# Performance work log

Hardware: AMD Instinct MI355X
Metric: run time of the kernel (lower is better)

Reference implementation:

```python
import jax, jax.numpy as jnp
import numpy as np

NEG_SLOPE = 0.2


def edge_softmax(logits, dst, num_nodes):
    # logits: [E, H]; softmax over edges grouped by destination node
    m = jax.ops.segment_max(logits, dst, num_segments=num_nodes)
    e = jnp.exp(logits - m[dst])
    s = jax.ops.segment_sum(e, dst, num_segments=num_nodes)
    return e / (s[dst] + 1e-16)


def gat_conv(x, edge_index, Wl, Wr, att, bias, We=None, eattr=None):
    # GATv2-style multi-head conv; heads concatenated. No dropout (eval mode).
    N = x.shape[0]
    H, C = att.shape
    xl = (x @ Wl).reshape(N, H, C)
    xr = (x @ Wr).reshape(N, H, C)
    src, dst = edge_index[0], edge_index[1]
    m = xl[src] + xr[dst]                      # [E, H, C]
    if eattr is not None:
        m = m + (eattr @ We).reshape(-1, H, C)
    logits = jnp.einsum('ehc,hc->eh', jax.nn.leaky_relu(m, NEG_SLOPE), att)
    alpha = edge_softmax(logits, dst, N)       # [E, H]
    out = jax.ops.segment_sum(alpha[..., None] * xl[src], dst, num_segments=N)
    return out.reshape(N, H * C) + bias


def layer_norm(h, gamma, beta, eps=1e-5):
    mu = jnp.mean(h, axis=-1, keepdims=True)
    var = jnp.var(h, axis=-1, keepdims=True)
    return (h - mu) * jax.lax.rsqrt(var + eps) * gamma + beta


def setup_inputs() -> dict:
    key = jax.random.key(0)
    N, E, D = 50000, 500000, 128
    H, C = 16, 8
    ks = jax.random.split(key, 32)
    inp = {
        'x': jax.random.normal(ks[0], (N, D), jnp.float32),
        'edge_index': jax.random.randint(ks[1], (2, E), 0, N),
        'edge_index_d2': jax.random.randint(ks[2], (2, E), 0, N),
        'edge_index_d4': jax.random.randint(ks[3], (2, E // 2), 0, N),
        'edge_index_d8': jax.random.randint(ks[4], (2, E // 4), 0, N),
        'dual_attr': jax.random.normal(ks[5], (E, D), jnp.float32),
        'edge_attr': jax.random.normal(ks[6], (E, D), jnp.float32),
        'oemap_idx': jax.random.randint(ks[7], (400000,), 0, E + 1),
    }
    s = 1.0 / np.sqrt(D)
    i = 8
    for c in (1, 2, 3, 4):
        inp[f'Wl{c}'] = jax.random.normal(ks[i], (D, H * C), jnp.float32) * s; i += 1
        inp[f'Wr{c}'] = jax.random.normal(ks[i], (D, H * C), jnp.float32) * s; i += 1
        inp[f'att{c}'] = jax.random.normal(ks[i], (H, C), jnp.float32) * s; i += 1
        inp[f'b{c}'] = jnp.zeros((H * C,), jnp.float32)
    inp['We1'] = jax.random.normal(ks[i], (D, H * C), jnp.float32) * s; i += 1
    inp['fuse_W'] = jax.random.normal(ks[i], (4 * H * C, D), jnp.float32) / np.sqrt(4 * H * C); i += 1
    inp['fuse_b'] = jnp.zeros((D,), jnp.float32)
    inp['ln_g'] = jnp.ones((2 * D,), jnp.float32)
    inp['ln_b'] = jnp.zeros((2 * D,), jnp.float32)
    inp['mlp_W'] = jax.random.normal(ks[i], (2 * D, D), jnp.float32) / np.sqrt(2 * D); i += 1
    inp['mlp_b'] = jnp.zeros((D,), jnp.float32)
    return inp


def reference(x, edge_index, edge_index_d2, edge_index_d4, edge_index_d8,
              dual_attr, edge_attr, oemap_idx,
              Wl1, Wr1, att1, b1, Wl2, Wr2, att2, b2,
              Wl3, Wr3, att3, b3, Wl4, Wr4, att4, b4,
              We1, fuse_W, fuse_b, ln_g, ln_b, mlp_W, mlp_b):
    x1 = gat_conv(x, edge_index, Wl1, Wr1, att1, b1, We1, dual_attr)
    x2 = gat_conv(x, edge_index_d2, Wl2, Wr2, att2, b2)
    x3 = gat_conv(x, edge_index_d4, Wl3, Wr3, att3, b3)
    x4 = gat_conv(x, edge_index_d8, Wl4, Wr4, att4, b4)
    xf = jnp.concatenate([x1, x2, x3, x4], axis=1) @ fuse_W + fuse_b  # [N, D]
    src, dst = edge_index[0], edge_index[1]
    pair = jnp.concatenate([xf[src], xf[dst]], axis=-1)               # [E, 2D]
    e_out = jax.nn.relu(layer_norm(pair, ln_g, ln_b)) @ mlp_W + mlp_b
    edge_attr_new = edge_attr + e_out
    # Node2EdgeNaiveReplace: pad with ones row, gather via oemap_idx
    padded = jnp.concatenate([edge_attr_new, jnp.ones((1, edge_attr_new.shape[1]), edge_attr_new.dtype)], axis=0)
    dual_out = padded[oemap_idx]
    return (xf, edge_attr_new, dual_out)
```

## Files before the change

### kernel.cpp

```cpp
#include <hip/hip_runtime.h>
#include <cstdint>
#include <cstddef>


#define NEG_SLOPE 0.2f

__device__ __forceinline__ unsigned fenc(float f) {
  unsigned u = __float_as_uint(f);
  return (u & 0x80000000u) ? ~u : (u | 0x80000000u);
}
__device__ __forceinline__ float fdec(unsigned k) {
  unsigned u = (k & 0x80000000u) ? (k & 0x7FFFFFFFu) : ~k;
  return __uint_as_float(u);
}

__global__ __launch_bounds__(128) void gemm_rows8_128(
    const float* __restrict__ A, const float* __restrict__ W,
    const float* __restrict__ biasA, float* __restrict__ out,
    int M, int accumulate)
{
  __shared__ __align__(16) float lds[8 * 128];
  const int t = threadIdx.x;
  const int row0 = blockIdx.x * 8;
#pragma unroll
  for (int r = 0; r < 8; ++r) {
    int row = row0 + r;
    float v = 0.f;
    if (row < M) {
      v = A[(size_t)row * 128 + t];
      if (biasA) v += biasA[t];
    }
    lds[r * 128 + t] = v;
  }
  __syncthreads();
  float acc[8] = {0.f, 0.f, 0.f, 0.f, 0.f, 0.f, 0.f, 0.f};
  for (int k = 0; k < 128; k += 4) {
    float w0 = W[(k + 0) * 128 + t];
    float w1 = W[(k + 1) * 128 + t];
    float w2 = W[(k + 2) * 128 + t];
    float w3 = W[(k + 3) * 128 + t];
#pragma unroll
    for (int r = 0; r < 8; ++r) {
      const float4 v = *(const float4*)&lds[r * 128 + k];
      acc[r] += v.x * w0 + v.y * w1 + v.z * w2 + v.w * w3;
    }
  }
#pragma unroll
  for (int r = 0; r < 8; ++r) {
    int row = row0 + r;
    if (row < M) {
      size_t o = (size_t)row * 128 + t;
      out[o] = accumulate ? (out[o] + acc[r]) : acc[r];
    }
  }
}

__global__ __launch_bounds__(128) void logits_conv1(
    const float* __restrict__ xl, const float* __restrict__ xr,
    const int* __restrict__ src, const int* __restrict__ dst,
    const float* __restrict__ dualA, const float* __restrict__ We,
    const float* __restrict__ att,
    float* __restrict__ ebuf, unsigned* __restrict__ nmax, int E)
{
  __shared__ __align__(16) float lds[16 * 128];
  __shared__ int sidx[16], didx[16];
  const int t = threadIdx.x;
  const int e0 = blockIdx.x * 16;

  for (int r = 0; r < 16; ++r) {
    int e = e0 + r;
    lds[r * 128 + t] = (e < E) ? dualA[(size_t)e * 128 + t] : 0.f;
  }
  if (t < 16) {
    int e = e0 + t;
    sidx[t] = (e < E) ? src[e] : 0;
    didx[t] = (e < E) ? dst[e] : 0;
  }
  __syncthreads();

  float acc[16];
#pragma unroll
  for (int r = 0; r < 16; ++r) acc[r] = 0.f;
  for (int k = 0; k < 128; k += 4) {
    float w0 = We[(k + 0) * 128 + t];
    float w1 = We[(k + 1) * 128 + t];
    float w2 = We[(k + 2) * 128 + t];
    float w3 = We[(k + 3) * 128 + t];
#pragma unroll
    for (int r = 0; r < 16; ++r) {
      const float4 v = *(const float4*)&lds[r * 128 + k];
      acc[r] += v.x * w0 + v.y * w1 + v.z * w2 + v.w * w3;
    }
  }

  const float a_t = att[t];
  const int h = t >> 3;
  for (int r = 0; r < 16; ++r) {
    int e = e0 + r;
    if (e >= E) break;
    float m = acc[r] + xl[(size_t)sidx[r] * 128 + t] + xr[(size_t)didx[r] * 128 + t];
    float lr = (m > 0.f) ? m : NEG_SLOPE * m;
    float v = lr * a_t;
    v += __shfl_down(v, 4, 8);
    v += __shfl_down(v, 2, 8);
    v += __shfl_down(v, 1, 8);
    if ((t & 7) == 0) {
      ebuf[(size_t)e * 16 + h] = v;
      atomicMax(&nmax[(size_t)didx[r] * 16 + h], fenc(v));
    }
  }
}

__global__ __launch_bounds__(128) void logits_plain(
    const float* __restrict__ xl, const float* __restrict__ xr,
    const int* __restrict__ src, const int* __restrict__ dst,
    const float* __restrict__ att,
    float* __restrict__ ebuf, unsigned* __restrict__ nmax, int E)
{
  const int e = blockIdx.x;
  const int t = threadIdx.x;
  const int s = src[e], d = dst[e];
  float m = xl[(size_t)s * 128 + t] + xr[(size_t)d * 128 + t];
  float lr = (m > 0.f) ? m : NEG_SLOPE * m;
  float v = lr * att[t];
  v += __shfl_down(v, 4, 8);
  v += __shfl_down(v, 2, 8);
  v += __shfl_down(v, 1, 8);
  if ((t & 7) == 0) {
    int h = t >> 3;
    ebuf[(size_t)e * 16 + h] = v;
    atomicMax(&nmax[(size_t)d * 16 + h], fenc(v));
  }
}

__global__ __launch_bounds__(256) void exp_sum(
    const int* __restrict__ dst, float* __restrict__ ebuf,
    const unsigned* __restrict__ nmax, float* __restrict__ nsum, int E)
{
  int i = blockIdx.x * 256 + threadIdx.x;
  if (i >= E * 16) return;
  int e = i >> 4, h = i & 15;
  int d = dst[e];
  float m = fdec(nmax[(size_t)d * 16 + h]);
  float ex = expf(ebuf[i] - m);
  ebuf[i] = ex;
  atomicAdd(&nsum[(size_t)d * 16 + h], ex);
}

__global__ __launch_bounds__(256) void aggregate(
    const int* __restrict__ src, const int* __restrict__ dst,
    const float* __restrict__ ebuf, const float* __restrict__ nsum,
    const float* __restrict__ xl, float* __restrict__ xc, int E)
{
  long long i = (long long)blockIdx.x * 256 + threadIdx.x;
  if (i >= (long long)E * 128) return;
  int e = (int)(i >> 7), t = (int)(i & 127), h = t >> 3;
  int s = src[e], d = dst[e];
  float alpha = ebuf[(size_t)e * 16 + h] / (nsum[(size_t)d * 16 + h] + 1e-16f);
  atomicAdd(&xc[(size_t)d * 128 + t], alpha * xl[(size_t)s * 128 + t]);
}

__global__ __launch_bounds__(256) void init_xf(
    float* __restrict__ xf, const float* __restrict__ fb, int total)
{
  int i = blockIdx.x * 256 + threadIdx.x;
  if (i < total) xf[i] = fb[i & 127];
}

__global__ __launch_bounds__(128) void edge_mlp(
    const float* __restrict__ xf,
    const int* __restrict__ src, const int* __restrict__ dst,
    const float* __restrict__ ln_g, const float* __restrict__ ln_b,
    const float* __restrict__ mlpW, const float* __restrict__ mlp_b,
    const float* __restrict__ edge_attr, float* __restrict__ out, int E)
{
  __shared__ __align__(16) float lds[16 * 256];
  __shared__ int sidx[16], didx[16];
  const int t = threadIdx.x;
  const int e0 = blockIdx.x * 16;
  if (t < 16) {
    int e = e0 + t;
    sidx[t] = (e < E) ? src[e] : 0;
    didx[t] = (e < E) ? dst[e] : 0;
  }
  __syncthreads();
  for (int r = 0; r < 16; ++r) {
    int e = e0 + r;
    if (e < E) {
      lds[r * 256 + t]       = xf[(size_t)sidx[r] * 128 + t];
      lds[r * 256 + 128 + t] = xf[(size_t)didx[r] * 128 + t];
    } else {
      lds[r * 256 + t] = 0.f;
      lds[r * 256 + 128 + t] = 0.f;
    }
  }
  __syncthreads();

  {
    const int g = t >> 3, j = t & 7;
    float s = 0.f, sq = 0.f;
    for (int i = 0; i < 32; ++i) {
      float v = lds[g * 256 + j + 8 * i];
      s += v; sq += v * v;
    }
    for (int off = 4; off; off >>= 1) {
      s  += __shfl_down(s,  off, 8);
      sq += __shfl_down(sq, off, 8);
    }
    s  = __shfl(s, 0, 8);
    sq = __shfl(sq, 0, 8);
    float mu = s * (1.f / 256.f);
    float var = sq * (1.f / 256.f) - mu * mu;
    float rs = rsqrtf(var + 1e-5f);
    for (int i = 0; i < 32; ++i) {
      int idx = j + 8 * i;
      float v = lds[g * 256 + idx];
      v = (v - mu) * rs * ln_g[idx] + ln_b[idx];
      lds[g * 256 + idx] = v > 0.f ? v : 0.f;
    }
  }
  __syncthreads();

  float acc[16];
#pragma unroll
  for (int r = 0; r < 16; ++r) acc[r] = 0.f;
  for (int k = 0; k < 256; k += 4) {
    float w0 = mlpW[(k + 0) * 128 + t];
    float w1 = mlpW[(k + 1) * 128 + t];
    float w2 = mlpW[(k + 2) * 128 + t];
    float w3 = mlpW[(k + 3) * 128 + t];
#pragma unroll
    for (int r = 0; r < 16; ++r) {
      const float4 v = *(const float4*)&lds[r * 256 + k];
      acc[r] += v.x * w0 + v.y * w1 + v.z * w2 + v.w * w3;
    }
  }
  const float mb = mlp_b[t];
  for (int r = 0; r < 16; ++r) {
    int e = e0 + r;
    if (e < E)
      out[(size_t)e * 128 + t] = edge_attr[(size_t)e * 128 + t] + acc[r] + mb;
  }
}

__global__ __launch_bounds__(256) void gather_dual(
    const int* __restrict__ idx, const float* __restrict__ ean,
    float* __restrict__ out, int M, int E)
{
  long long i = (long long)blockIdx.x * 256 + threadIdx.x;
  if (i >= (long long)M * 128) return;
  int row = (int)(i >> 7), t = (int)(i & 127);
  int r = idx[row];
  out[i] = (r < E) ? ean[(size_t)r * 128 + t] : 1.0f;
}


extern "C" void kernel_launch(void* const* d_in, const int* in_sizes, int n_in,
                              void* d_out, int out_size, void* d_ws, size_t ws_size,
                              hipStream_t stream)
{
  const float* x         = (const float*)d_in[0];
  const int*   ei[4]     = {(const int*)d_in[1], (const int*)d_in[2],
                            (const int*)d_in[3], (const int*)d_in[4]};
  const float* dual_attr = (const float*)d_in[5];
  const float* edge_attr = (const float*)d_in[6];
  const int*   oemap     = (const int*)d_in[7];
  const float* Wl[4]  = {(const float*)d_in[8],  (const float*)d_in[12],
                         (const float*)d_in[16], (const float*)d_in[20]};
  const float* Wr[4]  = {(const float*)d_in[9],  (const float*)d_in[13],
                         (const float*)d_in[17], (const float*)d_in[21]};
  const float* att[4] = {(const float*)d_in[10], (const float*)d_in[14],
                         (const float*)d_in[18], (const float*)d_in[22]};
  const float* bc[4]  = {(const float*)d_in[11], (const float*)d_in[15],
                         (const float*)d_in[19], (const float*)d_in[23]};
  const float* We1    = (const float*)d_in[24];
  const float* fuse_W = (const float*)d_in[25];
  const float* fuse_b = (const float*)d_in[26];
  const float* ln_g   = (const float*)d_in[27];
  const float* ln_b   = (const float*)d_in[28];
  const float* mlp_W  = (const float*)d_in[29];
  const float* mlp_b  = (const float*)d_in[30];

  const int N  = in_sizes[0] / 128;
  int E[4];
  for (int c = 0; c < 4; ++c) E[c] = in_sizes[1 + c] / 2;
  const int Moe = in_sizes[7];

  float* ws    = (float*)d_ws;
  float* xl    = ws;
  float* xr    = xl + (size_t)N * 128;
  float* xc    = xr + (size_t)N * 128;
  float* ebuf  = xc + (size_t)N * 128;
  unsigned* nmax = (unsigned*)(ebuf + (size_t)E[0] * 16);
  float* nsum  = (float*)(nmax + (size_t)N * 16);

  float* xf      = (float*)d_out;
  float* ean     = xf + (size_t)N * 128;
  float* dualout = ean + (size_t)E[0] * 128;

  const int rowBlocks = (N + 7) / 8;

  init_xf<<<(N * 128 + 255) / 256, 256, 0, stream>>>(xf, fuse_b, N * 128);

  for (int c = 0; c < 4; ++c) {
    const int* src = ei[c];
    const int* dst = ei[c] + E[c];

    gemm_rows8_128<<<rowBlocks, 128, 0, stream>>>(x, Wl[c], nullptr, xl, N, 0);
    gemm_rows8_128<<<rowBlocks, 128, 0, stream>>>(x, Wr[c], nullptr, xr, N, 0);

    hipMemsetAsync(xc,   0, (size_t)N * 128 * sizeof(float), stream);
    hipMemsetAsync(nmax, 0, (size_t)N * 16 * sizeof(unsigned), stream);
    hipMemsetAsync(nsum, 0, (size_t)N * 16 * sizeof(float), stream);

    if (c == 0) {
      logits_conv1<<<(E[c] + 15) / 16, 128, 0, stream>>>(
          xl, xr, src, dst, dual_attr, We1, att[c], ebuf, nmax, E[c]);
    } else {
      logits_plain<<<E[c], 128, 0, stream>>>(
          xl, xr, src, dst, att[c], ebuf, nmax, E[c]);
    }

    exp_sum<<<(E[c] * 16 + 255) / 256, 256, 0, stream>>>(dst, ebuf, nmax, nsum, E[c]);

    aggregate<<<(int)(((long long)E[c] * 128 + 255) / 256), 256, 0, stream>>>(
        src, dst, ebuf, nsum, xl, xc, E[c]);

    gemm_rows8_128<<<rowBlocks, 128, 0, stream>>>(
        xc, fuse_W + (size_t)c * 128 * 128, bc[c], xf, N, 1);
  }

  edge_mlp<<<(E[0] + 15) / 16, 128, 0, stream>>>(
      xf, ei[0], ei[0] + E[0], ln_g, ln_b, mlp_W, mlp_b, edge_attr, ean, E[0]);

  gather_dual<<<(int)(((long long)Moe * 128 + 255) / 256), 256, 0, stream>>>(
      oemap, ean, dualout, Moe, E[0]);
}
```

Measured before the change: 3.748 ms.

## Use split-bf16 MFMA for node GEMMs and edge MLP with prepacked weights

Replaces the scalar FP32 GEMMs (node projections, fuse projection) and the edge MLP with MFMA bf16 kernels. Each value is split into high and low bf16 parts and three MFMAs are accumulated to keep near-FP32 accuracy. Weights are prepacked once per call into the MFMA fragment layout in workspace. The edge MLP now loads gathered rows as float4 and computes LayerNorm per edge with 4 lanes. The cost is three times the MFMA work, an extra pack kernel, and accuracy that is slightly below full FP32.

Measured after the change: 3.202 ms. 1.17x faster.

```diff
diff --git a/kernel.cpp b/kernel.cpp
--- a/kernel.cpp
+++ b/kernel.cpp
@@ -5,6 +5,9 @@
 
 #define NEG_SLOPE 0.2f
 
+typedef __attribute__((ext_vector_type(8))) short short8v;
+typedef __attribute__((ext_vector_type(4))) float f32x4v;
+
 __device__ __forceinline__ unsigned fenc(float f) {
   unsigned u = __float_as_uint(f);
   return (u & 0x80000000u) ? ~u : (u | 0x80000000u);
@@ -14,43 +17,190 @@
   return __uint_as_float(u);
 }
 
-__global__ __launch_bounds__(128) void gemm_rows8_128(
-    const float* __restrict__ A, const float* __restrict__ W,
+__device__ __forceinline__ void cvt_bf16x2(float f, short& h, short& l) {
+  unsigned u = __float_as_uint(f);
+  h = (short)(u >> 16);
+  float fh = __uint_as_float(u & 0xFFFF0000u);
+  l = (short)(__float_as_uint(f - fh) >> 16);
+}
+
+struct PackArgs { const float* w[13]; };
+
+__global__ __launch_bounds__(256) void pack_all(PackArgs pa, short* __restrict__ out)
+{
+  const int seg = blockIdx.y;
+  const int K = (seg == 12) ? 256 : 128;
+  const int total = K * 128;
+  int i = blockIdx.x * 256 + threadIdx.x;
+  if (i >= total) return;
+  int j  = i & 7;
+  int l  = (i >> 3) & 63;
+  int ct = (i >> 9) & 7;
+  int s  = i >> 12;
+  int row = s * 32 + (l >> 4) * 8 + j;
+  int col = ct * 16 + (l & 15);
+  float v = pa.w[seg][row * 128 + col];
+  short h, lo;
+  cvt_bf16x2(v, h, lo);
+  short* oseg = out + (size_t)seg * 32768;
+  oseg[i] = h;
+  oseg[total + i] = lo;
+}
+
+__global__ __launch_bounds__(128) void gemm_mfma_n(
+    const float* __restrict__ A, const short* __restrict__ Wp,
     const float* __restrict__ biasA, float* __restrict__ out,
     int M, int accumulate)
 {
-  __shared__ __align__(16) float lds[8 * 128];
+  __shared__ __align__(16) short Ah[32][136];
+  __shared__ __align__(16) short Al[32][136];
   const int t = threadIdx.x;
-  const int row0 = blockIdx.x * 8;
-#pragma unroll
-  for (int r = 0; r < 8; ++r) {
+  const int row0 = blockIdx.x * 32;
+
+  const int cg = t & 31, rg = t >> 5;
+  float4 b4 = make_float4(0.f, 0.f, 0.f, 0.f);
+  if (biasA) b4 = *(const float4*)&biasA[cg * 4];
+#pragma unroll
+  for (int rr = 0; rr < 8; ++rr) {
+    int r = rr * 4 + rg;
     int row = row0 + r;
-    float v = 0.f;
-    if (row < M) {
-      v = A[(size_t)row * 128 + t];
-      if (biasA) v += biasA[t];
-    }
-    lds[r * 128 + t] = v;
+    float4 v = make_float4(0.f, 0.f, 0.f, 0.f);
+    if (row < M) v = *(const float4*)&A[(size_t)row * 128 + cg * 4];
+    v.x += b4.x; v.y += b4.y; v.z += b4.z; v.w += b4.w;
+    short h0, h1, h2, h3, l0, l1, l2, l3;
+    cvt_bf16x2(v.x, h0, l0); cvt_bf16x2(v.y, h1, l1);
+    cvt_bf16x2(v.z, h2, l2); cvt_bf16x2(v.w, h3, l3);
+    *(short4*)&Ah[r][cg * 4] = make_short4(h0, h1, h2, h3);
+    *(short4*)&Al[r][cg * 4] = make_short4(l0, l1, l2, l3);
   }
   __syncthreads();
-  float acc[8] = {0.f, 0.f, 0.f, 0.f, 0.f, 0.f, 0.f, 0.f};
-  for (int k = 0; k < 128; k += 4) {
-    float w0 = W[(k + 0) * 128 + t];
-    float w1 = W[(k + 1) * 128 + t];
-    float w2 = W[(k + 2) * 128 + t];
-    float w3 = W[(k + 3) * 128 + t];
-#pragma unroll
-    for (int r = 0; r < 8; ++r) {
-      const float4 v = *(const float4*)&lds[r * 128 + k];
-      acc[r] += v.x * w0 + v.y * w1 + v.z * w2 + v.w * w3;
-    }
-  }
-#pragma unroll
-  for (int r = 0; r < 8; ++r) {
-    int row = row0 + r;
-    if (row < M) {
-      size_t o = (size_t)row * 128 + t;
-      out[o] = accumulate ? (out[o] + acc[r]) : acc[r];
+
+  const int l = t & 63, w = t >> 6;
+  const int lr = l & 15, lg = l >> 4;
+  f32x4v acc[8] = {};
+  const short* WpLo = Wp + 128 * 128;
+#pragma unroll
+  for (int s = 0; s < 4; ++s) {
+    short8v ah = *(const short8v*)&Ah[w * 16 + lr][s * 32 + lg * 8];
+    short8v al = *(const short8v*)&Al[w * 16 + lr][s * 32 + lg * 8];
+#pragma unroll
+    for (int ct = 0; ct < 8; ++ct) {
+      int fo = ((s * 8 + ct) * 64 + l) * 8;
+      short8v wh = *(const short8v*)(Wp + fo);
+      short8v wl = *(const short8v*)(WpLo + fo);
+      acc[ct] = __builtin_amdgcn_mfma_f32_16x16x32_bf16(ah, wh, acc[ct], 0, 0, 0);
+      acc[ct] = __builtin_amdgcn_mfma_f32_16x16x32_bf16(al, wh, acc[ct], 0, 0, 0);
+      acc[ct] = __builtin_amdgcn_mfma_f32_16x16x32_bf16(ah, wl, acc[ct], 0, 0, 0);
+    }
+  }
+#pragma unroll
+  for (int ct = 0; ct < 8; ++ct) {
+#pragma unroll
+    for (int q = 0; q < 4; ++q) {
+      int row = row0 + w * 16 + lg * 4 + q;
+      if (row < M) {
+        size_t o = (size_t)row * 128 + ct * 16 + lr;
+        float v = acc[ct][q];
+        out[o] = accumulate ? (out[o] + v) : v;
+      }
+    }
+  }
+}
+
+__global__ __launch_bounds__(128) void edge_mlp_mfma(
+    const float* __restrict__ xf,
+    const int* __restrict__ src, const int* __restrict__ dst,
+    const float* __restrict__ ln_g, const float* __restrict__ ln_b,
+    const short* __restrict__ Wp, const float* __restrict__ mlp_b,
+    const float* __restrict__ edge_attr, float* __restrict__ out, int E)
+{
+  __shared__ __align__(16) short Ah[32][264];
+  __shared__ __align__(16) short Al[32][264];
+  __shared__ float sg[256], sb[256];
+  __shared__ int sidx[32], didx[32];
+  const int t = threadIdx.x;
+  const int e0 = blockIdx.x * 32;
+
+  if (t < 32) {
+    int e = e0 + t;
+    sidx[t] = (e < E) ? src[e] : src[0];
+    didx[t] = (e < E) ? dst[e] : dst[0];
+  }
+  sg[t] = ln_g[t];       sg[128 + t] = ln_g[128 + t];
+  sb[t] = ln_b[t];       sb[128 + t] = ln_b[128 + t];
+  __syncthreads();
+
+  const int r = t >> 2, j = t & 3;
+  const float* prs = xf + (size_t)sidx[r] * 128;
+  const float* prd = xf + (size_t)didx[r] * 128;
+  float4 va[8], vb[8];
+#pragma unroll
+  for (int m = 0; m < 8; ++m) {
+    va[m] = *(const float4*)(prs + (m * 4 + j) * 4);
+    vb[m] = *(const float4*)(prd + (m * 4 + j) * 4);
+  }
+  float s1 = 0.f, s2 = 0.f;
+#pragma unroll
+  for (int m = 0; m < 8; ++m) {
+    s1 += va[m].x + va[m].y + va[m].z + va[m].w;
+    s1 += vb[m].x + vb[m].y + vb[m].z + vb[m].w;
+    s2 += va[m].x * va[m].x + va[m].y * va[m].y + va[m].z * va[m].z + va[m].w * va[m].w;
+    s2 += vb[m].x * vb[m].x + vb[m].y * vb[m].y + vb[m].z * vb[m].z + vb[m].w * vb[m].w;
+  }
+  s1 += __shfl_xor(s1, 1); s1 += __shfl_xor(s1, 2);
+  s2 += __shfl_xor(s2, 1); s2 += __shfl_xor(s2, 2);
+  const float mu = s1 * (1.f / 256.f);
+  const float var = s2 * (1.f / 256.f) - mu * mu;
+  const float rs = rsqrtf(var + 1e-5f);
+
+#pragma unroll
+  for (int m = 0; m < 8; ++m) {
+    const int c4 = (m * 4 + j) * 4;
+#pragma unroll
+    for (int half = 0; half < 2; ++half) {
+      const float4 v = half ? vb[m] : va[m];
+      const int k = half * 128 + c4;
+      float el[4] = {v.x, v.y, v.z, v.w};
+      short h[4], lo[4];
+#pragma unroll
+      for (int u = 0; u < 4; ++u) {
+        float f = (el[u] - mu) * rs * sg[k + u] + sb[k + u];
+        f = f > 0.f ? f : 0.f;
+        cvt_bf16x2(f, h[u], lo[u]);
+      }
+      *(short4*)&Ah[r][k] = make_short4(h[0], h[1], h[2], h[3]);
+      *(short4*)&Al[r][k] = make_short4(lo[0], lo[1], lo[2], lo[3]);
+    }
+  }
+  __syncthreads();
+
+  const int l = t & 63, w = t >> 6;
+  const int lr = l & 15, lg = l >> 4;
+  f32x4v acc[8] = {};
+  const short* WpLo = Wp + 256 * 128;
+  for (int s = 0; s < 8; ++s) {
+    short8v ah = *(const short8v*)&Ah[w * 16 + lr][s * 32 + lg * 8];
+    short8v al = *(const short8v*)&Al[w * 16 + lr][s * 32 + lg * 8];
+#pragma unroll
+    for (int ct = 0; ct < 8; ++ct) {
+      int fo = ((s * 8 + ct) * 64 + l) * 8;
+      short8v wh = *(const short8v*)(Wp + fo);
+      short8v wl = *(const short8v*)(WpLo + fo);
+      acc[ct] = __builtin_amdgcn_mfma_f32_16x16x32_bf16(ah, wh, acc[ct], 0, 0, 0);
+      acc[ct] = __builtin_amdgcn_mfma_f32_16x16x32_bf16(al, wh, acc[ct], 0, 0, 0);
+      acc[ct] = __builtin_amdgcn_mfma_f32_16x16x32_bf16(ah, wl, acc[ct], 0, 0, 0);
+    }
+  }
+#pragma unroll
+  for (int ct = 0; ct < 8; ++ct) {
+    const int col = ct * 16 + lr;
+    const float mb = mlp_b[col];
+#pragma unroll
+    for (int q = 0; q < 4; ++q) {
+      int e = e0 + w * 16 + lg * 4 + q;
+      if (e < E)
+        out[(size_t)e * 128 + col] =
+            edge_attr[(size_t)e * 128 + col] + acc[ct][q] + mb;
     }
   }
 }
@@ -165,82 +315,6 @@
 {
   int i = blockIdx.x * 256 + threadIdx.x;
   if (i < total) xf[i] = fb[i & 127];
-}
-
-__global__ __launch_bounds__(128) void edge_mlp(
-    const float* __restrict__ xf,
-    const int* __restrict__ src, const int* __restrict__ dst,
-    const float* __restrict__ ln_g, const float* __restrict__ ln_b,
-    const float* __restrict__ mlpW, const float* __restrict__ mlp_b,
-    const float* __restrict__ edge_attr, float* __restrict__ out, int E)
-{
-  __shared__ __align__(16) float lds[16 * 256];
-  __shared__ int sidx[16], didx[16];
-  const int t = threadIdx.x;
-  const int e0 = blockIdx.x * 16;
-  if (t < 16) {
-    int e = e0 + t;
-    sidx[t] = (e < E) ? src[e] : 0;
-    didx[t] = (e < E) ? dst[e] : 0;
-  }
-  __syncthreads();
-  for (int r = 0; r < 16; ++r) {
-    int e = e0 + r;
-    if (e < E) {
-      lds[r * 256 + t]       = xf[(size_t)sidx[r] * 128 + t];
-      lds[r * 256 + 128 + t] = xf[(size_t)didx[r] * 128 + t];
-    } else {
-      lds[r * 256 + t] = 0.f;
-      lds[r * 256 + 128 + t] = 0.f;
-    }
-  }
-  __syncthreads();
-
-  {
-    const int g = t >> 3, j = t & 7;
-    float s = 0.f, sq = 0.f;
-    for (int i = 0; i < 32; ++i) {
-      float v = lds[g * 256 + j + 8 * i];
-      s += v; sq += v * v;
-    }
-    for (int off = 4; off; off >>= 1) {
-      s  += __shfl_down(s,  off, 8);
-      sq += __shfl_down(sq, off, 8);
-    }
-    s  = __shfl(s, 0, 8);
-    sq = __shfl(sq, 0, 8);
-    float mu = s * (1.f / 256.f);
-    float var = sq * (1.f / 256.f) - mu * mu;
-    float rs = rsqrtf(var + 1e-5f);
-    for (int i = 0; i < 32; ++i) {
-      int idx = j + 8 * i;
-      float v = lds[g * 256 + idx];
-      v = (v - mu) * rs * ln_g[idx] + ln_b[idx];
-      lds[g * 256 + idx] = v > 0.f ? v : 0.f;
-    }
-  }
-  __syncthreads();
-
-  float acc[16];
-#pragma unroll
-  for (int r = 0; r < 16; ++r) acc[r] = 0.f;
-  for (int k = 0; k < 256; k += 4) {
-    float w0 = mlpW[(k + 0) * 128 + t];
-    float w1 = mlpW[(k + 1) * 128 + t];
-    float w2 = mlpW[(k + 2) * 128 + t];
-    float w3 = mlpW[(k + 3) * 128 + t];
-#pragma unroll
-    for (int r = 0; r < 16; ++r) {
-      const float4 v = *(const float4*)&lds[r * 256 + k];
-      acc[r] += v.x * w0 + v.y * w1 + v.z * w2 + v.w * w3;
-    }
-  }
-  const float mb = mlp_b[t];
-  for (int r = 0; r < 16; ++r) {
-    int e = e0 + r;
-    if (e < E)
-      out[(size_t)e * 128 + t] = edge_attr[(size_t)e * 128 + t] + acc[r] + mb;
-  }
 }
 
 __global__ __launch_bounds__(256) void gather_dual(
@@ -286,7 +360,8 @@
   for (int c = 0; c < 4; ++c) E[c] = in_sizes[1 + c] / 2;
   const int Moe = in_sizes[7];
 
-  float* ws    = (float*)d_ws;
+  short* wp = (short*)d_ws;
+  float* ws = (float*)(wp + 458752);
   float* xl    = ws;
   float* xr    = xl + (size_t)N * 128;
   float* xc    = xr + (size_t)N * 128;
@@ -298,7 +373,16 @@
   float* ean     = xf + (size_t)N * 128;
   float* dualout = ean + (size_t)E[0] * 128;
 
-  const int rowBlocks = (N + 7) / 8;
+  const int rowBlocks32 = (N + 31) / 32;
+
+  PackArgs pa;
+  for (int c = 0; c < 4; ++c) {
+    pa.w[c]     = Wl[c];
+    pa.w[4 + c] = Wr[c];
+    pa.w[8 + c] = fuse_W + (size_t)c * 128 * 128;
+  }
+  pa.w[12] = mlp_W;
+  pack_all<<<dim3(128, 13), 256, 0, stream>>>(pa, wp);
 
   init_xf<<<(N * 128 + 255) / 256, 256, 0, stream>>>(xf, fuse_b, N * 128);
 
@@ -306,8 +390,10 @@
     const int* src = ei[c];
     const int* dst = ei[c] + E[c];
 
-    gemm_rows8_128<<<rowBlocks, 128, 0, stream>>>(x, Wl[c], nullptr, xl, N, 0);
-    gemm_rows8_128<<<rowBlocks, 128, 0, stream>>>(x, Wr[c], nullptr, xr, N, 0);
+    gemm_mfma_n<<<rowBlocks32, 128, 0, stream>>>(
+        x, wp + (size_t)c * 32768, nullptr, xl, N, 0);
+    gemm_mfma_n<<<rowBlocks32, 128, 0, stream>>>(
+        x, wp + (size_t)(4 + c) * 32768, nullptr, xr, N, 0);
 
     hipMemsetAsync(xc,   0, (size_t)N * 128 * sizeof(float), stream);
     hipMemsetAsync(nmax, 0, (size_t)N * 16 * sizeof(unsigned), stream);
@@ -326,12 +412,13 @@
     aggregate<<<(int)(((long long)E[c] * 128 + 255) / 256), 256, 0, stream>>>(
         src, dst, ebuf, nsum, xl, xc, E[c]);
 
-    gemm_rows8_128<<<rowBlocks, 128, 0, stream>>>(
-        xc, fuse_W + (size_t)c * 128 * 128, bc[c], xf, N, 1);
-  }
-
-  edge_mlp<<<(E[0] + 15) / 16, 128, 0, stream>>>(
-      xf, ei[0], ei[0] + E[0], ln_g, ln_b, mlp_W, mlp_b, edge_attr, ean, E[0]);
+    gemm_mfma_n<<<rowBlocks32, 128, 0, stream>>>(
+        xc, wp + (size_t)(8 + c) * 32768, bc[c], xf, N, 1);
+  }
+
+  edge_mlp_mfma<<<(E[0] + 31) / 32, 128, 0, stream>>>(
+      xf, ei[0], ei[0] + E[0], ln_g, ln_b, wp + 12 * 32768, mlp_b,
+      edge_attr, ean, E[0]);
 
   gather_dual<<<(int)(((long long)Moe * 128 + 255) / 256), 256, 0, stream>>>(
       oemap, ean, dualout, Moe, E[0]);
```
